# Optimization experiments

Measured on AMD Instinct MI355X. Metric: run time of the kernel, lower is better.

Reference implementation:

```python
import jax, jax.numpy as jnp
import numpy as np

UNITS = 512

def setup_inputs() -> dict:
    key = jax.random.key(0)
    ks = jax.random.split(key, 7)
    B, T, D, U = 64, 2048, 256, UNITS
    return {
        "x":   jax.random.normal(ks[0], (B, T, D), dtype=jnp.float32),
        "Wk":  jax.random.normal(ks[1], (D, 2 * U), dtype=jnp.float32) * 0.05,
        "Wrk": jax.random.normal(ks[2], (U, 2 * U), dtype=jnp.float32) * 0.05,
        "brk": jnp.zeros((2 * U,), dtype=jnp.float32),
        "Wu":  jax.random.normal(ks[3], (D, U), dtype=jnp.float32) * 0.05,
        "Wur": jax.random.normal(ks[4], (U, U), dtype=jnp.float32) * 0.05,
        "bur": jnp.zeros((U,), dtype=jnp.float32),
    }

def reference(x, Wk, Wrk, brk, Wu, Wur, bur):
    B, T, D = x.shape
    U = Wu.shape[1]
    # Precompute all input projections in two batched GEMMs (fuse over time).
    xz = jnp.einsum('btd,dk->btk', x, Wk)   # [B, T, 2U]
    xu = jnp.einsum('btd,du->btu', x, Wu)   # [B, T, U]
    h0 = jnp.zeros((B, U), dtype=x.dtype)

    def step(h, inp):
        xz_t, xu_t = inp                      # [B,2U], [B,U]
        z = xz_t + h @ Wrk + brk              # [B, 2U]
        r_t = jax.nn.sigmoid(z[:, :U])
        z_t = jax.nn.sigmoid(z[:, U:])
        h_t = jnp.tanh(xu_t + (h * r_t) @ Wur + bur)
        h_new = (1.0 - z_t) * h + z_t * h_t
        return h_new, None

    # scan over time axis
    xz_t = jnp.swapaxes(xz, 0, 1)  # [T, B, 2U]
    xu_t = jnp.swapaxes(xu, 0, 1)  # [T, B, U]
    h_final, _ = jax.lax.scan(step, h0, (xz_t, xu_t))
    return h_final  # [B, U] — original returns stacked states sliced to last step
```

## Files before the change

kernel.cpp:

```cpp
#include <hip/hip_runtime.h>


#define TT 2048
#define DD 256
#define UU 512

typedef short bf16x8 __attribute__((ext_vector_type(8)));
typedef float f32x4 __attribute__((ext_vector_type(4)));
typedef unsigned int u32;
typedef unsigned long long u64;

#define H_OFF 0
#define HR_OFF 131072
#define FLAG_OFF 262144
#define WS_BYTES 266240

__device__ inline unsigned short f2bf(float f) {
  unsigned u = __builtin_bit_cast(unsigned, f);
  u += 0x7FFFu + ((u >> 16) & 1u);
  return (unsigned short)(u >> 16);
}
__device__ inline float bf2f(unsigned short b) {
  unsigned u = ((unsigned)b) << 16;
  return __builtin_bit_cast(float, u);
}
__device__ inline u32 ld_coh_u32(const u32* p) {
  return __hip_atomic_load(p, __ATOMIC_RELAXED, __HIP_MEMORY_SCOPE_AGENT);
}
__device__ inline u64 ld_coh_u64(const u64* p) {
  return __hip_atomic_load(p, __ATOMIC_RELAXED, __HIP_MEMORY_SCOPE_AGENT);
}
__device__ inline void st_coh_u32(u32* p, u32 v) {
  __hip_atomic_store(p, v, __ATOMIC_RELAXED, __HIP_MEMORY_SCOPE_AGENT);
}

#define MFMA(A, B, C) __builtin_amdgcn_mfma_f32_16x16x32_bf16((A), (B), (C), 0, 0, 0)

__global__ __launch_bounds__(256, 1) void gru_persist(
    const float* __restrict__ x, const float* __restrict__ Wk,
    const float* __restrict__ Wrk, const float* __restrict__ brk,
    const float* __restrict__ Wu, const float* __restrict__ Wur,
    const float* __restrict__ bur, float* __restrict__ out,
    unsigned char* __restrict__ ws) {
  __shared__ float scratch[24576];

  const int wg = blockIdx.x;
  const int bblk = wg & 3;
  const int cb = wg >> 2;
  const bool zwg = (cb >= 32);
  const int tid = threadIdx.x;
  const int lane = tid & 63;
  const int wv = tid >> 6;
  const int kgrp = lane >> 4;
  const int c = lane & 15;

  const int P1C0 = cb * 16;
  const int P2C0 = zwg ? (cb - 32) * 16 : 0;

  u32* h_pack = (u32*)(ws + H_OFF);
  u32* hr_pack = (u32*)(ws + HR_OFF);
  u32* flags = (u32*)(ws + FLAG_OFF) + bblk * 256;

  bf16x8 w1hi[6], w1lo[6], w2hi[6], w2lo[6];
#pragma unroll
  for (int j = 0; j < 6; ++j) {
    const int kb = (wv + 4 * j) * 32 + kgrp * 8;
#pragma unroll
    for (int i = 0; i < 8; ++i) {
      const int k = kb + i;
      float v = (k < DD) ? Wk[(size_t)k * 1024 + P1C0 + c]
                         : Wrk[(size_t)(k - DD) * 1024 + P1C0 + c];
      unsigned short hb = f2bf(v);
      w1hi[j][i] = (short)hb;
      w1lo[j][i] = (short)f2bf(v - bf2f(hb));
      float v2 = 0.f;
      if (zwg)
        v2 = (k < DD) ? Wu[(size_t)k * UU + P2C0 + c]
                      : Wur[(size_t)(k - DD) * UU + P2C0 + c];
      unsigned short hb2 = f2bf(v2);
      w2hi[j][i] = (short)hb2;
      w2lo[j][i] = (short)f2bf(v2 - bf2f(hb2));
    }
  }

  const int bl = tid >> 4, cl = tid & 15;
  const int Bg = bblk * 16 + bl;
  const float b1 = brk[P1C0 + cl];
  const float b2 = zwg ? bur[P2C0 + cl] : 0.f;

  const int rowb = bblk * 16 + c;

  bf16x8 xhi[2], xlo[2];
  auto split_x = [&](int t) {
#pragma unroll
    for (int j = 0; j < 2; ++j) {
      const float* xr =
          x + ((size_t)rowb * TT + t) * DD + wv * 32 + j * 128 + kgrp * 8;
      f32x4 v0 = *(const f32x4*)(xr);
      f32x4 v1 = *(const f32x4*)(xr + 4);
#pragma unroll
      for (int i = 0; i < 4; ++i) {
        unsigned short hb = f2bf(v0[i]);
        xhi[j][i] = (short)hb;
        xlo[j][i] = (short)f2bf(v0[i] - bf2f(hb));
        unsigned short hb2 = f2bf(v1[i]);
        xhi[j][4 + i] = (short)hb2;
        xlo[j][4 + i] = (short)f2bf(v1[i] - bf2f(hb2));
      }
    }
  };
  split_x(0);

  auto gemm = [&](const u32* pack, const bf16x8* whi,
                  const bf16x8* wlo) -> f32x4 {
    u64 q[4][4];
#pragma unroll
    for (int j = 0; j < 4; ++j) {
      const int k0 = wv * 32 + j * 128 + kgrp * 8;
      const u64* src = (const u64*)(pack + (size_t)rowb * UU + k0);
      q[j][0] = ld_coh_u64(src + 0);
      q[j][1] = ld_coh_u64(src + 1);
      q[j][2] = ld_coh_u64(src + 2);
      q[j][3] = ld_coh_u64(src + 3);
    }
    f32x4 a0 = {0.f, 0.f, 0.f, 0.f}, a1 = {0.f, 0.f, 0.f, 0.f};
    a0 = MFMA(xhi[0], whi[0], a0);
    a0 = MFMA(xhi[0], wlo[0], a0);
    a0 = MFMA(xlo[0], whi[0], a0);
    a1 = MFMA(xhi[1], whi[1], a1);
    a1 = MFMA(xhi[1], wlo[1], a1);
    a1 = MFMA(xlo[1], whi[1], a1);
#pragma unroll
    for (int j = 0; j < 4; ++j) {
      bf16x8 ahi, alo;
#pragma unroll
      for (int i = 0; i < 4; ++i) {
        u32 lo32 = (u32)q[j][i];
        u32 hi32 = (u32)(q[j][i] >> 32);
        ahi[2 * i] = (short)(lo32 >> 16);
        alo[2 * i] = (short)lo32;
        ahi[2 * i + 1] = (short)(hi32 >> 16);
        alo[2 * i + 1] = (short)hi32;
      }
      if ((j & 1) == 0) {
        a0 = MFMA(ahi, whi[j + 2], a0);
        a0 = MFMA(ahi, wlo[j + 2], a0);
        a0 = MFMA(alo, whi[j + 2], a0);
      } else {
        a1 = MFMA(ahi, whi[j + 2], a1);
        a1 = MFMA(ahi, wlo[j + 2], a1);
        a1 = MFMA(alo, whi[j + 2], a1);
      }
    }
    return a0 + a1;
  };

  unsigned bar = 0;
  for (int t = 0; t < TT; ++t) {
    u32 hp = 0;
    if (!zwg) hp = ld_coh_u32(h_pack + (size_t)Bg * UU + P1C0 + cl);
    f32x4 acc = gemm(h_pack, w1hi, w1lo);
#pragma unroll
    for (int r = 0; r < 4; ++r)
      scratch[wv * 256 + (kgrp * 4 + r) * 16 + c] = acc[r];
    __syncthreads();
    {
      float z = (scratch[tid] + scratch[256 + tid]) +
                (scratch[512 + tid] + scratch[768 + tid]) + b1;
      float s = 1.f / (1.f + __expf(-z));
      if (!zwg) {
        float h = bf2f((unsigned short)(hp >> 16)) + bf2f((unsigned short)hp);
        float hrv = h * s;
        unsigned short hb = f2bf(hrv);
        unsigned short lb = f2bf(hrv - bf2f(hb));
        st_coh_u32(hr_pack + (size_t)Bg * UU + P1C0 + cl,
                   ((u32)hb << 16) | lb);
      }
      float zt = s;

      asm volatile("s_waitcnt vmcnt(0)" ::: "memory");
      __syncthreads();
      ++bar;
      if (tid == 0) st_coh_u32(flags + cb * 4, bar);
      if (wv == 0) {
        const u32* fp = flags + lane * 4;
        while (!__all(ld_coh_u32(fp) >= bar)) {
        }
      }
      __syncthreads();

      if (zwg) {
        u32 hp2 = ld_coh_u32(h_pack + (size_t)Bg * UU + P2C0 + cl);
        f32x4 acc2 = gemm(hr_pack, w2hi, w2lo);
#pragma unroll
        for (int r = 0; r < 4; ++r)
          scratch[wv * 256 + (kgrp * 4 + r) * 16 + c] = acc2[r];
        __syncthreads();
        float u = (scratch[tid] + scratch[256 + tid]) +
                  (scratch[512 + tid] + scratch[768 + tid]) + b2;
        float e = __expf(2.f * u);
        float ht = 1.f - 2.f / (e + 1.f);
        float ho = bf2f((unsigned short)(hp2 >> 16)) + bf2f((unsigned short)hp2);
        float hn = ho + zt * (ht - ho);
        unsigned short hb = f2bf(hn);
        unsigned short lb = f2bf(hn - bf2f(hb));
        st_coh_u32(h_pack + (size_t)Bg * UU + P2C0 + cl, ((u32)hb << 16) | lb);
        if (t == TT - 1) out[(size_t)Bg * UU + P2C0 + cl] = hn;
      }

      asm volatile("s_waitcnt vmcnt(0)" ::: "memory");
      __syncthreads();
      ++bar;
      if (tid == 0) st_coh_u32(flags + cb * 4, bar);
      if (t + 1 < TT) split_x(t + 1);
      if (wv == 0) {
        const u32* fp = flags + lane * 4;
        while (!__all(ld_coh_u32(fp) >= bar)) {
        }
      }
      __syncthreads();
    }
  }
}

extern "C" void kernel_launch(void* const* d_in, const int* in_sizes, int n_in,
                              void* d_out, int out_size, void* d_ws,
                              size_t ws_size, hipStream_t stream) {
  (void)in_sizes; (void)n_in; (void)out_size; (void)ws_size;
  hipMemsetAsync(d_ws, 0, WS_BYTES, stream);
  gru_persist<<<dim3(256), dim3(256), 0, stream>>>(
      (const float*)d_in[0], (const float*)d_in[1], (const float*)d_in[2],
      (const float*)d_in[3], (const float*)d_in[4], (const float*)d_in[5],
      (const float*)d_in[6], (float*)d_out, (unsigned char*)d_ws);
}
```

Before: 16.41 ms.

## Replace grid flag barriers with per-element step tags and double-buffered state

Drops the two global flag barriers per timestep. Each hidden-state and reset-gated value is now stored as a 64-bit word carrying the timestep tag, and the h and h*r buffers are double-buffered by step parity. Consumers poll their own input chunks until every tag matches, so each workgroup waits only on the data it needs rather than on all workgroups. This also lets the x-projection MFMAs and the next x split overlap the waits. In exchange the state traffic doubles in bytes and many lanes spin on global memory.

New measurement: 30.08 ms. +83.3%, slower.

```diff
diff --git a/kernel.cpp b/kernel.cpp
--- a/kernel.cpp
+++ b/kernel.cpp
@@ -10,10 +10,9 @@
 typedef unsigned int u32;
 typedef unsigned long long u64;
 
-#define H_OFF 0
-#define HR_OFF 131072
-#define FLAG_OFF 262144
-#define WS_BYTES 266240
+#define H2_OFF 0
+#define HR2_OFF 524288
+#define WS_BYTES 1048576
 
 __device__ inline unsigned short f2bf(float f) {
   unsigned u = __builtin_bit_cast(unsigned, f);
@@ -24,13 +23,10 @@
   unsigned u = ((unsigned)b) << 16;
   return __builtin_bit_cast(float, u);
 }
-__device__ inline u32 ld_coh_u32(const u32* p) {
-  return __hip_atomic_load(p, __ATOMIC_RELAXED, __HIP_MEMORY_SCOPE_AGENT);
-}
 __device__ inline u64 ld_coh_u64(const u64* p) {
   return __hip_atomic_load(p, __ATOMIC_RELAXED, __HIP_MEMORY_SCOPE_AGENT);
 }
-__device__ inline void st_coh_u32(u32* p, u32 v) {
+__device__ inline void st_coh_u64(u64* p, u64 v) {
   __hip_atomic_store(p, v, __ATOMIC_RELAXED, __HIP_MEMORY_SCOPE_AGENT);
 }
 
@@ -57,9 +53,8 @@
   const int P1C0 = cb * 16;
   const int P2C0 = zwg ? (cb - 32) * 16 : 0;
 
-  u32* h_pack = (u32*)(ws + H_OFF);
-  u32* hr_pack = (u32*)(ws + HR_OFF);
-  u32* flags = (u32*)(ws + FLAG_OFF) + bblk * 256;
+  u64* h2 = (u64*)(ws + H2_OFF);
+  u64* hr2 = (u64*)(ws + HR2_OFF);
 
   bf16x8 w1hi[6], w1lo[6], w2hi[6], w2lo[6];
 #pragma unroll
@@ -109,116 +104,131 @@
       }
     }
   };
+
+  auto poll_chunk = [&](const u64* p, u32 exp, bf16x8& AHI, bf16x8& ALO) {
+    u64 q0, q1, q2, q3, q4, q5, q6, q7;
+    for (;;) {
+      q0 = ld_coh_u64(p + 0); q1 = ld_coh_u64(p + 1);
+      q2 = ld_coh_u64(p + 2); q3 = ld_coh_u64(p + 3);
+      q4 = ld_coh_u64(p + 4); q5 = ld_coh_u64(p + 5);
+      q6 = ld_coh_u64(p + 6); q7 = ld_coh_u64(p + 7);
+      int ok = ((u32)q0 == exp) & ((u32)q1 == exp) & ((u32)q2 == exp) &
+               ((u32)q3 == exp) & ((u32)q4 == exp) & ((u32)q5 == exp) &
+               ((u32)q6 == exp) & ((u32)q7 == exp);
+      if (__all(ok)) break;
+      __builtin_amdgcn_s_sleep(1);
+    }
+    u32 w;
+    w = (u32)(q0 >> 32); AHI[0] = (short)(w >> 16); ALO[0] = (short)w;
+    w = (u32)(q1 >> 32); AHI[1] = (short)(w >> 16); ALO[1] = (short)w;
+    w = (u32)(q2 >> 32); AHI[2] = (short)(w >> 16); ALO[2] = (short)w;
+    w = (u32)(q3 >> 32); AHI[3] = (short)(w >> 16); ALO[3] = (short)w;
+    w = (u32)(q4 >> 32); AHI[4] = (short)(w >> 16); ALO[4] = (short)w;
+    w = (u32)(q5 >> 32); AHI[5] = (short)(w >> 16); ALO[5] = (short)w;
+    w = (u32)(q6 >> 32); AHI[6] = (short)(w >> 16); ALO[6] = (short)w;
+    w = (u32)(q7 >> 32); AHI[7] = (short)(w >> 16); ALO[7] = (short)w;
+  };
+
   split_x(0);
 
-  auto gemm = [&](const u32* pack, const bf16x8* whi,
-                  const bf16x8* wlo) -> f32x4 {
-    u64 q[4][4];
-#pragma unroll
-    for (int j = 0; j < 4; ++j) {
-      const int k0 = wv * 32 + j * 128 + kgrp * 8;
-      const u64* src = (const u64*)(pack + (size_t)rowb * UU + k0);
-      q[j][0] = ld_coh_u64(src + 0);
-      q[j][1] = ld_coh_u64(src + 1);
-      q[j][2] = ld_coh_u64(src + 2);
-      q[j][3] = ld_coh_u64(src + 3);
-    }
+  for (int t = 0; t < TT; ++t) {
+    const u32 exp_h = (u32)t;
+    const u64* hrow = h2 + ((size_t)((t + 1) & 1) * 64 + rowb) * 512;
+
     f32x4 a0 = {0.f, 0.f, 0.f, 0.f}, a1 = {0.f, 0.f, 0.f, 0.f};
-    a0 = MFMA(xhi[0], whi[0], a0);
-    a0 = MFMA(xhi[0], wlo[0], a0);
-    a0 = MFMA(xlo[0], whi[0], a0);
-    a1 = MFMA(xhi[1], whi[1], a1);
-    a1 = MFMA(xhi[1], wlo[1], a1);
-    a1 = MFMA(xlo[1], whi[1], a1);
-#pragma unroll
-    for (int j = 0; j < 4; ++j) {
+    a0 = MFMA(xhi[0], w1hi[0], a0);
+    a0 = MFMA(xhi[0], w1lo[0], a0);
+    a0 = MFMA(xlo[0], w1hi[0], a0);
+    a1 = MFMA(xhi[1], w1hi[1], a1);
+    a1 = MFMA(xhi[1], w1lo[1], a1);
+    a1 = MFMA(xlo[1], w1hi[1], a1);
+#pragma unroll
+    for (int j = 2; j < 6; ++j) {
+      const int kh = 32 * (wv + 4 * j - 8) + kgrp * 8;
       bf16x8 ahi, alo;
-#pragma unroll
-      for (int i = 0; i < 4; ++i) {
-        u32 lo32 = (u32)q[j][i];
-        u32 hi32 = (u32)(q[j][i] >> 32);
-        ahi[2 * i] = (short)(lo32 >> 16);
-        alo[2 * i] = (short)lo32;
-        ahi[2 * i + 1] = (short)(hi32 >> 16);
-        alo[2 * i + 1] = (short)hi32;
-      }
+      poll_chunk(hrow + kh, exp_h, ahi, alo);
       if ((j & 1) == 0) {
-        a0 = MFMA(ahi, whi[j + 2], a0);
-        a0 = MFMA(ahi, wlo[j + 2], a0);
-        a0 = MFMA(alo, whi[j + 2], a0);
+        a0 = MFMA(ahi, w1hi[j], a0);
+        a0 = MFMA(ahi, w1lo[j], a0);
+        a0 = MFMA(alo, w1hi[j], a0);
       } else {
-        a1 = MFMA(ahi, whi[j + 2], a1);
-        a1 = MFMA(ahi, wlo[j + 2], a1);
-        a1 = MFMA(alo, whi[j + 2], a1);
-      }
-    }
-    return a0 + a1;
-  };
-
-  unsigned bar = 0;
-  for (int t = 0; t < TT; ++t) {
-    u32 hp = 0;
-    if (!zwg) hp = ld_coh_u32(h_pack + (size_t)Bg * UU + P1C0 + cl);
-    f32x4 acc = gemm(h_pack, w1hi, w1lo);
-#pragma unroll
-    for (int r = 0; r < 4; ++r)
-      scratch[wv * 256 + (kgrp * 4 + r) * 16 + c] = acc[r];
+        a1 = MFMA(ahi, w1hi[j], a1);
+        a1 = MFMA(ahi, w1lo[j], a1);
+        a1 = MFMA(alo, w1hi[j], a1);
+      }
+    }
+    {
+      f32x4 acc = a0 + a1;
+#pragma unroll
+      for (int r = 0; r < 4; ++r)
+        scratch[wv * 256 + (kgrp * 4 + r) * 16 + c] = acc[r];
+    }
     __syncthreads();
-    {
-      float z = (scratch[tid] + scratch[256 + tid]) +
-                (scratch[512 + tid] + scratch[768 + tid]) + b1;
-      float s = 1.f / (1.f + __expf(-z));
-      if (!zwg) {
-        float h = bf2f((unsigned short)(hp >> 16)) + bf2f((unsigned short)hp);
-        float hrv = h * s;
-        unsigned short hb = f2bf(hrv);
-        unsigned short lb = f2bf(hrv - bf2f(hb));
-        st_coh_u32(hr_pack + (size_t)Bg * UU + P1C0 + cl,
-                   ((u32)hb << 16) | lb);
-      }
-      float zt = s;
-
-      asm volatile("s_waitcnt vmcnt(0)" ::: "memory");
+    const float zsum = (scratch[tid] + scratch[256 + tid]) +
+                       (scratch[512 + tid] + scratch[768 + tid]) + b1;
+    const float s = 1.f / (1.f + __expf(-zsum));
+
+    if (!zwg) {
+      u64 hp = ld_coh_u64(h2 + ((size_t)((t + 1) & 1) * 64 + Bg) * 512 +
+                          P1C0 + cl);
+      u32 hw = (u32)(hp >> 32);
+      float h = bf2f((unsigned short)(hw >> 16)) + bf2f((unsigned short)hw);
+      float hrv = h * s;
+      unsigned short hb = f2bf(hrv);
+      unsigned short lb = f2bf(hrv - bf2f(hb));
+      u64 pv = (((u64)(((u32)hb << 16) | lb)) << 32) | (u32)(t + 1);
+      st_coh_u64(hr2 + ((size_t)(t & 1) * 64 + Bg) * 512 + P1C0 + cl, pv);
+      if (t + 1 < TT) split_x(t + 1);
+    } else {
+      const float zt = s;
+      f32x4 u0 = {0.f, 0.f, 0.f, 0.f}, u1 = {0.f, 0.f, 0.f, 0.f};
+      u0 = MFMA(xhi[0], w2hi[0], u0);
+      u0 = MFMA(xhi[0], w2lo[0], u0);
+      u0 = MFMA(xlo[0], w2hi[0], u0);
+      u1 = MFMA(xhi[1], w2hi[1], u1);
+      u1 = MFMA(xhi[1], w2lo[1], u1);
+      u1 = MFMA(xlo[1], w2hi[1], u1);
       __syncthreads();
-      ++bar;
-      if (tid == 0) st_coh_u32(flags + cb * 4, bar);
-      if (wv == 0) {
-        const u32* fp = flags + lane * 4;
-        while (!__all(ld_coh_u32(fp) >= bar)) {
+      if (t + 1 < TT) split_x(t + 1);
+
+      const u32 exp_hr = (u32)(t + 1);
+      const u64* hrrow = hr2 + ((size_t)(t & 1) * 64 + rowb) * 512;
+#pragma unroll
+      for (int j = 2; j < 6; ++j) {
+        const int kh = 32 * (wv + 4 * j - 8) + kgrp * 8;
+        bf16x8 ahi, alo;
+        poll_chunk(hrrow + kh, exp_hr, ahi, alo);
+        if ((j & 1) == 0) {
+          u0 = MFMA(ahi, w2hi[j], u0);
+          u0 = MFMA(ahi, w2lo[j], u0);
+          u0 = MFMA(alo, w2hi[j], u0);
+        } else {
+          u1 = MFMA(ahi, w2hi[j], u1);
+          u1 = MFMA(ahi, w2lo[j], u1);
+          u1 = MFMA(alo, w2hi[j], u1);
         }
       }
+      {
+        f32x4 acc = u0 + u1;
+#pragma unroll
+        for (int r = 0; r < 4; ++r)
+          scratch[wv * 256 + (kgrp * 4 + r) * 16 + c] = acc[r];
+      }
       __syncthreads();
-
-      if (zwg) {
-        u32 hp2 = ld_coh_u32(h_pack + (size_t)Bg * UU + P2C0 + cl);
-        f32x4 acc2 = gemm(hr_pack, w2hi, w2lo);
-#pragma unroll
-        for (int r = 0; r < 4; ++r)
-          scratch[wv * 256 + (kgrp * 4 + r) * 16 + c] = acc2[r];
-        __syncthreads();
-        float u = (scratch[tid] + scratch[256 + tid]) +
-                  (scratch[512 + tid] + scratch[768 + tid]) + b2;
-        float e = __expf(2.f * u);
-        float ht = 1.f - 2.f / (e + 1.f);
-        float ho = bf2f((unsigned short)(hp2 >> 16)) + bf2f((unsigned short)hp2);
-        float hn = ho + zt * (ht - ho);
-        unsigned short hb = f2bf(hn);
-        unsigned short lb = f2bf(hn - bf2f(hb));
-        st_coh_u32(h_pack + (size_t)Bg * UU + P2C0 + cl, ((u32)hb << 16) | lb);
-        if (t == TT - 1) out[(size_t)Bg * UU + P2C0 + cl] = hn;
-      }
-
-      asm volatile("s_waitcnt vmcnt(0)" ::: "memory");
-      __syncthreads();
-      ++bar;
-      if (tid == 0) st_coh_u32(flags + cb * 4, bar);
-      if (t + 1 < TT) split_x(t + 1);
-      if (wv == 0) {
-        const u32* fp = flags + lane * 4;
-        while (!__all(ld_coh_u32(fp) >= bar)) {
-        }
-      }
-      __syncthreads();
+      const float usum = (scratch[tid] + scratch[256 + tid]) +
+                         (scratch[512 + tid] + scratch[768 + tid]) + b2;
+      const float e = __expf(2.f * usum);
+      const float ht = 1.f - 2.f / (e + 1.f);
+      u64 hp2 = ld_coh_u64(h2 + ((size_t)((t + 1) & 1) * 64 + Bg) * 512 +
+                           P2C0 + cl);
+      u32 hw2 = (u32)(hp2 >> 32);
+      float ho = bf2f((unsigned short)(hw2 >> 16)) + bf2f((unsigned short)hw2);
+      float hn = ho + zt * (ht - ho);
+      unsigned short hb = f2bf(hn);
+      unsigned short lb = f2bf(hn - bf2f(hb));
+      u64 pv = (((u64)(((u32)hb << 16) | lb)) << 32) | (u32)(t + 1);
+      st_coh_u64(h2 + ((size_t)(t & 1) * 64 + Bg) * 512 + P2C0 + cl, pv);
+      if (t == TT - 1) out[(size_t)Bg * UU + P2C0 + cl] = hn;
     }
   }
 }
```

## Repartition GRU persistent kernel into 8 batch groups with per-wave flags

Applied to the files above, without the earlier changes.

Reorganizes the persistent GRU so each workgroup owns 16 hidden columns for all three gates (r, z, u) over an 8-row batch group, instead of splitting r/z and u gates across different workgroups. Synchronization is now among 32 workgroups per batch group using per-wave flags with sleep-polling, and h/hr state is double-buffered to avoid a second barrier. The input-projection MFMAs are hoisted off the critical path, overlapping the polls, and the low bf16 weight halves move to LDS. This trades more per-step work per workgroup and LDS reads for smaller sync groups and shorter dependency chains, but half the MFMA rows (8 of 16 batch rows) are redundant.

After: 14.57 ms, median of 2. -11.2%, faster.

```diff
diff --git a/kernel.cpp b/kernel.cpp
--- a/kernel.cpp
+++ b/kernel.cpp
@@ -10,10 +10,10 @@
 typedef unsigned int u32;
 typedef unsigned long long u64;
 
-#define H_OFF 0
-#define HR_OFF 131072
-#define FLAG_OFF 262144
-#define WS_BYTES 266240
+#define H2_OFF 0
+#define HR2_OFF 262144
+#define FLAG_OFF 524288
+#define WS_BYTES 557056
 
 __device__ inline unsigned short f2bf(float f) {
   unsigned u = __builtin_bit_cast(unsigned, f);
@@ -42,62 +42,80 @@
     const float* __restrict__ Wu, const float* __restrict__ Wur,
     const float* __restrict__ bur, float* __restrict__ out,
     unsigned char* __restrict__ ws) {
-  __shared__ float scratch[24576];
-
-  const int wg = blockIdx.x;
-  const int bblk = wg & 3;
-  const int cb = wg >> 2;
-  const bool zwg = (cb >= 32);
+  __shared__ short wlo[36864];
+  __shared__ float scratch[2304];
+
+  const int wgid = blockIdx.x;
+  const int g = wgid & 7;
+  const int rank = wgid >> 3;
   const int tid = threadIdx.x;
   const int lane = tid & 63;
   const int wv = tid >> 6;
   const int kgrp = lane >> 4;
   const int c = lane & 15;
 
-  const int P1C0 = cb * 16;
-  const int P2C0 = zwg ? (cb - 32) * 16 : 0;
-
-  u32* h_pack = (u32*)(ws + H_OFF);
-  u32* hr_pack = (u32*)(ws + HR_OFF);
-  u32* flags = (u32*)(ws + FLAG_OFF) + bblk * 256;
-
-  bf16x8 w1hi[6], w1lo[6], w2hi[6], w2lo[6];
+  const int C1 = 16 * rank;
+  const int C1z = 512 + C1;
+
+  bf16x8 wrhi[6], wzhi[6], wuhi[6];
 #pragma unroll
   for (int j = 0; j < 6; ++j) {
-    const int kb = (wv + 4 * j) * 32 + kgrp * 8;
+    const int kb = 32 * (wv + 4 * j) + kgrp * 8;
 #pragma unroll
     for (int i = 0; i < 8; ++i) {
       const int k = kb + i;
-      float v = (k < DD) ? Wk[(size_t)k * 1024 + P1C0 + c]
-                         : Wrk[(size_t)(k - DD) * 1024 + P1C0 + c];
-      unsigned short hb = f2bf(v);
-      w1hi[j][i] = (short)hb;
-      w1lo[j][i] = (short)f2bf(v - bf2f(hb));
-      float v2 = 0.f;
-      if (zwg)
-        v2 = (k < DD) ? Wu[(size_t)k * UU + P2C0 + c]
-                      : Wur[(size_t)(k - DD) * UU + P2C0 + c];
-      unsigned short hb2 = f2bf(v2);
-      w2hi[j][i] = (short)hb2;
-      w2lo[j][i] = (short)f2bf(v2 - bf2f(hb2));
-    }
-  }
+      float vr = (k < DD) ? Wk[(size_t)k * 1024 + C1 + c]
+                          : Wrk[(size_t)(k - DD) * 1024 + C1 + c];
+      float vz = (k < DD) ? Wk[(size_t)k * 1024 + C1z + c]
+                          : Wrk[(size_t)(k - DD) * 1024 + C1z + c];
+      float vu = (k < DD) ? Wu[(size_t)k * UU + C1 + c]
+                          : Wur[(size_t)(k - DD) * UU + C1 + c];
+      wrhi[j][i] = (short)f2bf(vr);
+      wzhi[j][i] = (short)f2bf(vz);
+      wuhi[j][i] = (short)f2bf(vu);
+    }
+  }
+  for (int idx = tid; idx < 3 * 12288; idx += 256) {
+    const int T = idx / 12288;
+    const int rem = idx - T * 12288;
+    const int k = rem >> 4, cc = rem & 15;
+    float v;
+    if (T == 0)
+      v = (k < DD) ? Wk[(size_t)k * 1024 + C1 + cc]
+                   : Wrk[(size_t)(k - DD) * 1024 + C1 + cc];
+    else if (T == 1)
+      v = (k < DD) ? Wk[(size_t)k * 1024 + C1z + cc]
+                   : Wrk[(size_t)(k - DD) * 1024 + C1z + cc];
+    else
+      v = (k < DD) ? Wu[(size_t)k * UU + C1 + cc]
+                   : Wur[(size_t)(k - DD) * UU + C1 + cc];
+    unsigned short hb = f2bf(v);
+    const int ch = k >> 5, kk = k & 31;
+    wlo[((T * 24 + ch) * 64 + (kk >> 3) * 16 + cc) * 8 + (kk & 7)] =
+        (short)f2bf(v - bf2f(hb));
+  }
+  __syncthreads();
+
+  u32* h2 = (u32*)(ws + H2_OFF);
+  u32* hr2 = (u32*)(ws + HR2_OFF);
+  u32* flg = (u32*)(ws + FLAG_OFF) + (size_t)g * 1024;
+  u32* myflag = flg + (rank * 2 + wv) * 16;
 
   const int bl = tid >> 4, cl = tid & 15;
-  const int Bg = bblk * 16 + bl;
-  const float b1 = brk[P1C0 + cl];
-  const float b2 = zwg ? bur[P2C0 + cl] : 0.f;
-
-  const int rowb = bblk * 16 + c;
+  const float b_r = brk[C1 + cl];
+  const float b_z = brk[C1z + cl];
+  const float b_u = bur[C1 + cl];
+
+  const int arow = c & 7;
+  const float* xrow = x + (size_t)(8 * g + arow) * TT * DD;
 
   bf16x8 xhi[2], xlo[2];
   auto split_x = [&](int t) {
 #pragma unroll
     for (int j = 0; j < 2; ++j) {
-      const float* xr =
-          x + ((size_t)rowb * TT + t) * DD + wv * 32 + j * 128 + kgrp * 8;
-      f32x4 v0 = *(const f32x4*)(xr);
-      f32x4 v1 = *(const f32x4*)(xr + 4);
+      const float* p = xrow + (size_t)t * DD + 32 * wv + 128 * j + kgrp * 8;
+      f32x4 v0 = *(const f32x4*)p;
+      f32x4 v1 = *(const f32x4*)(p + 4);
 #pragma unroll
       for (int i = 0; i < 4; ++i) {
         unsigned short hb = f2bf(v0[i]);
@@ -109,116 +127,151 @@
       }
     }
   };
+
+  auto poll = [&](u32 need) {
+    const u32* p = flg + lane * 16;
+    while (!__all(ld_coh_u32(p) >= need)) __builtin_amdgcn_s_sleep(1);
+  };
+
+  auto chunk3 = [&](const bf16x8& ahi, const bf16x8& alo, const bf16x8& bhi,
+                    const bf16x8& blo, f32x4& acc) {
+    acc = MFMA(ahi, bhi, acc);
+    acc = MFMA(ahi, blo, acc);
+    acc = MFMA(alo, bhi, acc);
+  };
+
   split_x(0);
-
-  auto gemm = [&](const u32* pack, const bf16x8* whi,
-                  const bf16x8* wlo) -> f32x4 {
-    u64 q[4][4];
-#pragma unroll
-    for (int j = 0; j < 4; ++j) {
-      const int k0 = wv * 32 + j * 128 + kgrp * 8;
-      const u64* src = (const u64*)(pack + (size_t)rowb * UU + k0);
-      q[j][0] = ld_coh_u64(src + 0);
-      q[j][1] = ld_coh_u64(src + 1);
-      q[j][2] = ld_coh_u64(src + 2);
-      q[j][3] = ld_coh_u64(src + 3);
-    }
-    f32x4 a0 = {0.f, 0.f, 0.f, 0.f}, a1 = {0.f, 0.f, 0.f, 0.f};
-    a0 = MFMA(xhi[0], whi[0], a0);
-    a0 = MFMA(xhi[0], wlo[0], a0);
-    a0 = MFMA(xlo[0], whi[0], a0);
-    a1 = MFMA(xhi[1], whi[1], a1);
-    a1 = MFMA(xhi[1], wlo[1], a1);
-    a1 = MFMA(xlo[1], whi[1], a1);
-#pragma unroll
-    for (int j = 0; j < 4; ++j) {
-      bf16x8 ahi, alo;
-#pragma unroll
-      for (int i = 0; i < 4; ++i) {
-        u32 lo32 = (u32)q[j][i];
-        u32 hi32 = (u32)(q[j][i] >> 32);
-        ahi[2 * i] = (short)(lo32 >> 16);
-        alo[2 * i] = (short)lo32;
-        ahi[2 * i + 1] = (short)(hi32 >> 16);
-        alo[2 * i + 1] = (short)hi32;
-      }
-      if ((j & 1) == 0) {
-        a0 = MFMA(ahi, whi[j + 2], a0);
-        a0 = MFMA(ahi, wlo[j + 2], a0);
-        a0 = MFMA(alo, whi[j + 2], a0);
-      } else {
-        a1 = MFMA(ahi, whi[j + 2], a1);
-        a1 = MFMA(ahi, wlo[j + 2], a1);
-        a1 = MFMA(alo, whi[j + 2], a1);
-      }
-    }
-    return a0 + a1;
-  };
-
-  unsigned bar = 0;
+  float hown = 0.f, zt_reg = 0.f;
+  f32x4 ar = {0.f, 0.f, 0.f, 0.f}, az = ar;
+#pragma unroll
+  for (int j = 0; j < 2; ++j) {
+    bf16x8 br = *(const bf16x8*)&wlo[((wv + 4 * j) * 64 + lane) * 8];
+    bf16x8 bz = *(const bf16x8*)&wlo[((24 + wv + 4 * j) * 64 + lane) * 8];
+    chunk3(xhi[0 + j], xlo[0 + j], wrhi[j], br, ar);
+    chunk3(xhi[0 + j], xlo[0 + j], wzhi[j], bz, az);
+  }
+
   for (int t = 0; t < TT; ++t) {
-    u32 hp = 0;
-    if (!zwg) hp = ld_coh_u32(h_pack + (size_t)Bg * UU + P1C0 + cl);
-    f32x4 acc = gemm(h_pack, w1hi, w1lo);
+    poll(2 * (u32)t);
+    {
+      const int bh = (t + 1) & 1;
+      const u64* hb = (const u64*)(h2 + ((size_t)(bh * 64 + 8 * g + arow)) * 512 +
+                                   32 * wv + kgrp * 8);
+      u64 Q[16];
+#pragma unroll
+      for (int p = 0; p < 4; ++p) {
+        Q[4 * p + 0] = ld_coh_u64(hb + 64 * p + 0);
+        Q[4 * p + 1] = ld_coh_u64(hb + 64 * p + 1);
+        Q[4 * p + 2] = ld_coh_u64(hb + 64 * p + 2);
+        Q[4 * p + 3] = ld_coh_u64(hb + 64 * p + 3);
+      }
+#pragma unroll
+      for (int p = 0; p < 4; ++p) {
+        bf16x8 ahi, alo;
+#pragma unroll
+        for (int i = 0; i < 4; ++i) {
+          u32 lo32 = (u32)Q[4 * p + i], hi32 = (u32)(Q[4 * p + i] >> 32);
+          ahi[2 * i] = (short)(lo32 >> 16);
+          alo[2 * i] = (short)lo32;
+          ahi[2 * i + 1] = (short)(hi32 >> 16);
+          alo[2 * i + 1] = (short)hi32;
+        }
+        const int j = p + 2;
+        bf16x8 br = *(const bf16x8*)&wlo[((wv + 4 * j) * 64 + lane) * 8];
+        bf16x8 bz = *(const bf16x8*)&wlo[((24 + wv + 4 * j) * 64 + lane) * 8];
+        chunk3(ahi, alo, wrhi[j], br, ar);
+        chunk3(ahi, alo, wzhi[j], bz, az);
+      }
+    }
+    __syncthreads();
+#pragma unroll
+    for (int r = 0; r < 4; ++r) {
+      scratch[wv * 256 + (kgrp * 4 + r) * 16 + c] = ar[r];
+      scratch[1024 + wv * 256 + (kgrp * 4 + r) * 16 + c] = az[r];
+    }
+    __syncthreads();
+    if (tid < 128) {
+      float rv = (scratch[tid] + scratch[256 + tid]) +
+                 (scratch[512 + tid] + scratch[768 + tid]) + b_r;
+      float zv = (scratch[1024 + tid] + scratch[1280 + tid]) +
+                 (scratch[1536 + tid] + scratch[1792 + tid]) + b_z;
+      float rg = 1.f / (1.f + __expf(-rv));
+      zt_reg = 1.f / (1.f + __expf(-zv));
+      float hrv = hown * rg;
+      unsigned short hb = f2bf(hrv);
+      unsigned short lb = f2bf(hrv - bf2f(hb));
+      st_coh_u32(hr2 + ((size_t)((t & 1) * 64 + 8 * g + bl)) * 512 + C1 + cl,
+                 ((u32)hb << 16) | lb);
+    }
+    asm volatile("s_waitcnt vmcnt(0)" ::: "memory");
+    if (wv < 2 && lane == 0) st_coh_u32(myflag, 2 * (u32)t + 1);
+
+    f32x4 au = {0.f, 0.f, 0.f, 0.f};
+#pragma unroll
+    for (int j = 0; j < 2; ++j) {
+      bf16x8 bu = *(const bf16x8*)&wlo[((48 + wv + 4 * j) * 64 + lane) * 8];
+      chunk3(xhi[j], xlo[j], wuhi[j], bu, au);
+    }
+    if (t + 1 < TT) split_x(t + 1);
+    poll(2 * (u32)t + 1);
+    {
+      const u64* hrb = (const u64*)(hr2 + ((size_t)((t & 1) * 64 + 8 * g + arow)) * 512 +
+                                    32 * wv + kgrp * 8);
+      u64 Q[16];
+#pragma unroll
+      for (int p = 0; p < 4; ++p) {
+        Q[4 * p + 0] = ld_coh_u64(hrb + 64 * p + 0);
+        Q[4 * p + 1] = ld_coh_u64(hrb + 64 * p + 1);
+        Q[4 * p + 2] = ld_coh_u64(hrb + 64 * p + 2);
+        Q[4 * p + 3] = ld_coh_u64(hrb + 64 * p + 3);
+      }
+#pragma unroll
+      for (int p = 0; p < 4; ++p) {
+        bf16x8 ahi, alo;
+#pragma unroll
+        for (int i = 0; i < 4; ++i) {
+          u32 lo32 = (u32)Q[4 * p + i], hi32 = (u32)(Q[4 * p + i] >> 32);
+          ahi[2 * i] = (short)(lo32 >> 16);
+          alo[2 * i] = (short)lo32;
+          ahi[2 * i + 1] = (short)(hi32 >> 16);
+          alo[2 * i + 1] = (short)hi32;
+        }
+        const int j = p + 2;
+        bf16x8 bu = *(const bf16x8*)&wlo[((48 + wv + 4 * j) * 64 + lane) * 8];
+        chunk3(ahi, alo, wuhi[j], bu, au);
+      }
+    }
+    __syncthreads();
 #pragma unroll
     for (int r = 0; r < 4; ++r)
-      scratch[wv * 256 + (kgrp * 4 + r) * 16 + c] = acc[r];
-    __syncthreads();
-    {
-      float z = (scratch[tid] + scratch[256 + tid]) +
-                (scratch[512 + tid] + scratch[768 + tid]) + b1;
-      float s = 1.f / (1.f + __expf(-z));
-      if (!zwg) {
-        float h = bf2f((unsigned short)(hp >> 16)) + bf2f((unsigned short)hp);
-        float hrv = h * s;
-        unsigned short hb = f2bf(hrv);
-        unsigned short lb = f2bf(hrv - bf2f(hb));
-        st_coh_u32(hr_pack + (size_t)Bg * UU + P1C0 + cl,
-                   ((u32)hb << 16) | lb);
-      }
-      float zt = s;
-
-      asm volatile("s_waitcnt vmcnt(0)" ::: "memory");
-      __syncthreads();
-      ++bar;
-      if (tid == 0) st_coh_u32(flags + cb * 4, bar);
-      if (wv == 0) {
-        const u32* fp = flags + lane * 4;
-        while (!__all(ld_coh_u32(fp) >= bar)) {
-        }
-      }
-      __syncthreads();
-
-      if (zwg) {
-        u32 hp2 = ld_coh_u32(h_pack + (size_t)Bg * UU + P2C0 + cl);
-        f32x4 acc2 = gemm(hr_pack, w2hi, w2lo);
-#pragma unroll
-        for (int r = 0; r < 4; ++r)
-          scratch[wv * 256 + (kgrp * 4 + r) * 16 + c] = acc2[r];
-        __syncthreads();
-        float u = (scratch[tid] + scratch[256 + tid]) +
-                  (scratch[512 + tid] + scratch[768 + tid]) + b2;
-        float e = __expf(2.f * u);
-        float ht = 1.f - 2.f / (e + 1.f);
-        float ho = bf2f((unsigned short)(hp2 >> 16)) + bf2f((unsigned short)hp2);
-        float hn = ho + zt * (ht - ho);
-        unsigned short hb = f2bf(hn);
-        unsigned short lb = f2bf(hn - bf2f(hb));
-        st_coh_u32(h_pack + (size_t)Bg * UU + P2C0 + cl, ((u32)hb << 16) | lb);
-        if (t == TT - 1) out[(size_t)Bg * UU + P2C0 + cl] = hn;
-      }
-
-      asm volatile("s_waitcnt vmcnt(0)" ::: "memory");
-      __syncthreads();
-      ++bar;
-      if (tid == 0) st_coh_u32(flags + cb * 4, bar);
-      if (t + 1 < TT) split_x(t + 1);
-      if (wv == 0) {
-        const u32* fp = flags + lane * 4;
-        while (!__all(ld_coh_u32(fp) >= bar)) {
-        }
-      }
-      __syncthreads();
+      scratch[wv * 256 + (kgrp * 4 + r) * 16 + c] = au[r];
+    __syncthreads();
+    if (tid < 128) {
+      float uv = (scratch[tid] + scratch[256 + tid]) +
+                 (scratch[512 + tid] + scratch[768 + tid]) + b_u;
+      float e = __expf(2.f * uv);
+      float th = 1.f - 2.f / (e + 1.f);
+      float hn = hown + zt_reg * (th - hown);
+      hown = hn;
+      unsigned short hb = f2bf(hn);
+      unsigned short lb = f2bf(hn - bf2f(hb));
+      st_coh_u32(h2 + ((size_t)((t & 1) * 64 + 8 * g + bl)) * 512 + C1 + cl,
+                 ((u32)hb << 16) | lb);
+      if (t == TT - 1) out[(size_t)(8 * g + bl) * UU + C1 + cl] = hn;
+    }
+    asm volatile("s_waitcnt vmcnt(0)" ::: "memory");
+    if (wv < 2 && lane == 0) st_coh_u32(myflag, 2 * (u32)t + 2);
+
+    ar = (f32x4){0.f, 0.f, 0.f, 0.f};
+    az = (f32x4){0.f, 0.f, 0.f, 0.f};
+    if (t + 1 < TT) {
+#pragma unroll
+      for (int j = 0; j < 2; ++j) {
+        bf16x8 br = *(const bf16x8*)&wlo[((wv + 4 * j) * 64 + lane) * 8];
+        bf16x8 bz = *(const bf16x8*)&wlo[((24 + wv + 4 * j) * 64 + lane) * 8];
+        chunk3(xhi[j], xlo[j], wrhi[j], br, ar);
+        chunk3(xhi[j], xlo[j], wzhi[j], bz, az);
+      }
     }
   }
 }
```
